# Performance work log

Measured on AMD Instinct MI355X. Metric: run time of the kernel, lower is better.

The kernel has to match this reference:

```python
import jax, jax.numpy as jnp
import numpy as np

QN, QP = -8.0, 7.0  # int4: Qn=-2**3, Qp=2**3-1
LOG2E = 1.4426950408889634  # 1/ln(2)

def round_ste(x):
    return x + jax.lax.stop_gradient(jnp.round(x) - x)

def sg(x):
    return jax.lax.stop_gradient(x)

def mean_var_int(x_int, scale=1024):
    """Serial integer running-mean/var recurrence over the last dim.
    x_int: (B,H,N,D) int32. Returns mu (int values, float32) and varn float32, shape (B,H,N,1).
    Matches the torch loop: m_i = m_{i-1} + (x_i-m_{i-1})*int(1024/(i+1))//1024,
    v_i = v_{i-1} + (x_i-m_{i-1})*(x_i-m_i), with m_0=x_0, v_0=0 (same as the general
    recurrence with m_{-1}=v_{-1}=0 since int(1024/1)=1024)."""
    D = x_int.shape[3]
    coef = jnp.array([scale // (i + 1) for i in range(D)], dtype=jnp.int32)
    xt = jnp.moveaxis(x_int, 3, 0)  # (D,B,H,N)
    z = jnp.zeros(x_int.shape[:3], jnp.int32)
    def step(carry, inp):
        m, v = carry
        xi, c = inp
        d = xi - m
        new_m = m + (d * c) // scale  # floor division, matches torch //
        new_v = v + d * (xi - new_m)
        return (new_m, new_v), None
    (m, v), _ = jax.lax.scan(step, (z, z), (xt, coef))
    mu = m[..., None].astype(jnp.float32)
    varn = v[..., None].astype(jnp.float32) / D
    return mu, varn

def q_attention_forward(x0, qkv_w, qkv_b, qkv_alpha, qkv_act_alpha,
                        proj_w, proj_b, proj_alpha, proj_act_alpha,
                        norm_q_w, norm_q_b, norm_k_w, norm_k_b,
                        q_alpha, k_alpha, v_alpha, attn_alpha,
                        num_heads=12):
    B, N, C = x0.shape
    H = num_heads
    hd = C // H
    head_scale = hd ** -0.5

    # input activation quantization (ActQ_v2 then .int())
    a_in = qkv_act_alpha.mean()
    x0_2b = sg(jnp.round(jnp.clip(x0 / a_in, QN, QP)))  # int-valued (B,N,C)

    # int4 qkv weight quantization (per-output-channel alpha), integer GEMM
    w_qkv = sg(jnp.round(jnp.clip(qkv_w / qkv_alpha[:, None], QN, QP)))  # (3C,C)
    qkv = jnp.einsum('bnc,oc->bno', x0_2b, w_qkv)
    bias_i = sg(jnp.trunc(qkv_b / a_in / qkv_alpha))  # bias.int()
    qkv = qkv + bias_i

    qkv = jnp.transpose(qkv.reshape(B, N, 3, H, hd), (2, 0, 3, 1, 4))
    q0, k0, v0 = qkv[0], qkv[1], qkv[2]  # (B,H,N,hd)
    alpha_r = qkv_alpha.reshape(3, H, 1, hd)

    # q branch: scaled integer mean/var norm + scaled quantization
    xq = q0 * alpha_r[0]
    mu_q, var_q = mean_var_int(xq.astype(jnp.int32))
    q1 = (xq - mu_q) / (jnp.sqrt(var_q) + 1e-5)
    aq = q_alpha.mean()
    q2 = sg(jnp.round(jnp.clip((q1 + norm_q_b / norm_q_w) * norm_q_w / aq, QN, QP)))

    # k branch
    xk = k0 * alpha_r[1]
    mu_k, var_k = mean_var_int(xk.astype(jnp.int32))
    k1 = (xk - mu_k) / (jnp.sqrt(var_k) + 1e-5)
    ak = k_alpha.mean()
    k2 = sg(jnp.round(jnp.clip((k1 + norm_k_b / norm_k_w) * norm_k_w / ak, QN, QP)))

    # v branch
    av = v_alpha.mean()
    v2 = sg(jnp.round(jnp.clip(v0 * (a_in * alpha_r[2]) / av, QN, QP)))

    # integer q @ k^T
    qk = jnp.einsum('bhqd,bhkd->bhqk', q2, k2)  # (B,H,N,N)

    # power-of-two softmax approximation: 2^floor(e) * (1 + frac(e))
    s = head_scale * aq * ak
    e = LOG2E * s * qk
    f = jnp.floor(e)
    attn_exp = jnp.exp2(f) * (1.0 + (e - f))
    am = attn_alpha.mean()
    attn_norm = attn_exp / attn_exp.sum(-1, keepdims=True)
    attn2 = sg(jnp.round(jnp.clip(attn_norm / am, QN, QP)))

    x1p = jnp.einsum('bhqk,bhkd->bhqd', attn2, v2)
    x1p = jnp.transpose(x1p, (0, 2, 1, 3)).reshape(B, N, C)

    # proj-act quantization (round_pass STE, no .int() here in torch)
    ap = proj_act_alpha.mean()
    x1_2b = round_ste(jnp.clip(x1p * (am * av) / ap, QN, QP))

    w_p = sg(jnp.round(jnp.clip(proj_w / proj_alpha[:, None], QN, QP)))  # w_q.int()
    x2 = jnp.einsum('bnc,oc->bno', x1_2b, w_p) * proj_alpha * ap + proj_b
    return x2

def setup_inputs() -> dict:
    key = jax.random.key(0)
    ks = jax.random.split(key, 17)
    B, N, C, H = 4, 1024, 768, 12
    u = lambda k, shape, lo, hi: jax.random.uniform(k, shape, jnp.float32, lo, hi)
    return {
        "x0": jax.random.normal(ks[0], (B, N, C), jnp.float32),
        "qkv_w": jax.random.normal(ks[1], (3 * C, C), jnp.float32) * 0.02,
        "qkv_b": jax.random.normal(ks[2], (3 * C,), jnp.float32),
        "qkv_alpha": u(ks[3], (3 * C,), 0.008, 0.012),
        "qkv_act_alpha": u(ks[4], (C,), 0.25, 0.35),
        "proj_w": jax.random.normal(ks[5], (C, C), jnp.float32) * 0.02,
        "proj_b": jax.random.normal(ks[6], (C,), jnp.float32) * 0.02,
        "proj_alpha": u(ks[7], (C,), 0.008, 0.012),
        "proj_act_alpha": u(ks[8], (C,), 0.008, 0.012),
        "norm_q_w": u(ks[9], (C // H,), 0.8, 1.2),
        "norm_q_b": jax.random.normal(ks[10], (C // H,), jnp.float32) * 0.1,
        "norm_k_w": u(ks[11], (C // H,), 0.8, 1.2),
        "norm_k_b": jax.random.normal(ks[12], (C // H,), jnp.float32) * 0.1,
        "q_alpha": u(ks[13], (H,), 0.25, 0.35),
        "k_alpha": u(ks[14], (H,), 0.25, 0.35),
        "v_alpha": u(ks[15], (H,), 0.15, 0.25),
        "attn_alpha": u(ks[16], (H,), 0.0008, 0.0015),
    }

def reference(x0, qkv_w, qkv_b, qkv_alpha, qkv_act_alpha,
              proj_w, proj_b, proj_alpha, proj_act_alpha,
              norm_q_w, norm_q_b, norm_k_w, norm_k_b,
              q_alpha, k_alpha, v_alpha, attn_alpha):
    return q_attention_forward(x0, qkv_w, qkv_b, qkv_alpha, qkv_act_alpha,
                               proj_w, proj_b, proj_alpha, proj_act_alpha,
                               norm_q_w, norm_q_b, norm_k_w, norm_k_b,
                               q_alpha, k_alpha, v_alpha, attn_alpha)
```

## Files before the change

### kernel.cpp

```cpp
#include <hip/hip_runtime.h>

typedef unsigned short u16;
typedef unsigned int u32;
typedef __attribute__((ext_vector_type(8))) u16 u16x8;
typedef __attribute__((ext_vector_type(8))) __bf16 bf16x8;
typedef __attribute__((ext_vector_type(4))) float f32x4;

#define LOG2E_F 1.4426950408889634f

__device__ __forceinline__ u16 f2bf(float f) {
  return (u16)(__float_as_uint(f) >> 16);
}
__device__ __forceinline__ float clip87(float x) {
  return fminf(fmaxf(x, -8.0f), 7.0f);
}

typedef const __attribute__((address_space(1))) u32* gp32;
typedef __attribute__((address_space(3))) u32* lp32;
__device__ __forceinline__ void gl16(const void* g, void* l) {
  __builtin_amdgcn_global_load_lds((gp32)g, (lp32)l, 16, 0, 0);
}

__global__ void k_scalars(const float* __restrict__ qkv_act_alpha,
                          const float* __restrict__ proj_act_alpha,
                          const float* __restrict__ q_alpha,
                          const float* __restrict__ k_alpha,
                          const float* __restrict__ v_alpha,
                          const float* __restrict__ attn_alpha,
                          float* __restrict__ scal) {
  int tid = threadIdx.x;
  int wave = tid >> 6, lane = tid & 63;
  if (wave < 6) {
    const float* src = nullptr; int n = 0;
    switch (wave) {
      case 0: src = qkv_act_alpha;  n = 768; break;
      case 1: src = q_alpha;        n = 12;  break;
      case 2: src = k_alpha;        n = 12;  break;
      case 3: src = v_alpha;        n = 12;  break;
      case 4: src = attn_alpha;     n = 12;  break;
      case 5: src = proj_act_alpha; n = 768; break;
    }
    double s = 0.0;
    for (int i = lane; i < n; i += 64) s += (double)src[i];
    s += __shfl_xor(s, 1);
    s += __shfl_xor(s, 2);
    s += __shfl_xor(s, 4);
    s += __shfl_xor(s, 8);
    s += __shfl_xor(s, 16);
    s += __shfl_xor(s, 32);
    if (lane == 0) scal[wave] = (float)(s / (double)n);
  }
  __syncthreads();
  if (tid == 0) {
    float aq = scal[1], ak = scal[2];
    float s_ = (0.125f * aq) * ak;
    scal[6] = LOG2E_F * s_;
    scal[7] = scal[4] * scal[3];
  }
}

__global__ __launch_bounds__(256) void k_quant_weights(
    const float* __restrict__ qkv_w, const float* __restrict__ qkv_alpha,
    const float* __restrict__ qkv_b, const float* __restrict__ proj_w,
    const float* __restrict__ proj_alpha, const float* __restrict__ scal,
    u16* __restrict__ wq, u16* __restrict__ wp, float* __restrict__ biasi) {
  int idx = blockIdx.x * 256 + threadIdx.x;
  const int T1 = 2304 * 768, T2 = 768 * 768;
  if (idx < T1) {
    int o = idx / 768;
    wq[idx] = f2bf(rintf(clip87(qkv_w[idx] / qkv_alpha[o])));
  } else if (idx < T1 + T2) {
    int j = idx - T1;
    int o = j / 768;
    wp[j] = f2bf(rintf(clip87(proj_w[j] / proj_alpha[o])));
  } else if (idx < T1 + T2 + 2304) {
    int o = idx - T1 - T2;
    biasi[o] = truncf((qkv_b[o] / scal[0]) / qkv_alpha[o]);
  }
}

__global__ __launch_bounds__(256) void k_quant_x0(const float* __restrict__ x0,
                                                  const float* __restrict__ scal,
                                                  u16* __restrict__ x0q) {
  int base = (blockIdx.x * 256 + threadIdx.x) * 8;
  float a = scal[0];
  f32x4 v0 = *(const f32x4*)&x0[base];
  f32x4 v1 = *(const f32x4*)&x0[base + 4];
  u16x8 o;
  #pragma unroll
  for (int j = 0; j < 4; j++) o[j] = f2bf(rintf(clip87(v0[j] / a)));
  #pragma unroll
  for (int j = 0; j < 4; j++) o[4 + j] = f2bf(rintf(clip87(v1[j] / a)));
  *(u16x8*)&x0q[base] = o;
}

__global__ __launch_bounds__(256) void k_gemm_qkv(
    const u16* __restrict__ A, const u16* __restrict__ Bt,
    const float* __restrict__ biasi, const float* __restrict__ qkv_alpha,
    const float* __restrict__ nqw, const float* __restrict__ nqb,
    const float* __restrict__ nkw, const float* __restrict__ nkb,
    const float* __restrict__ scal,
    u16* __restrict__ q2, u16* __restrict__ k2, u16* __restrict__ v2t) {
  const int K = 768;
  __shared__ __align__(16) float xt[128 * 129];
  u16* lA = (u16*)xt;
  u16* lB = ((u16*)xt) + 128 * 32;
  int tid = threadIdx.x;
  int lane = tid & 63, wave = tid >> 6;
  int wr = wave >> 1, wc = wave & 1;
  int m0 = blockIdx.y * 128, n0 = blockIdx.x * 128;

  f32x4 acc[4][4];
  #pragma unroll
  for (int mi = 0; mi < 4; mi++)
    #pragma unroll
    for (int ni = 0; ni < 4; ni++) acc[mi][ni] = (f32x4){0.f, 0.f, 0.f, 0.f};

  int srow = wave * 32 + (lane >> 2);
  int scol = (lane & 3) * 8;
  const u16* gA = A + (size_t)(m0 + srow) * K + scol;
  const u16* gB = Bt + (size_t)(n0 + srow) * K + scol;
  u16* lA0 = lA + wave * 2 * 512;
  u16* lB0 = lB + wave * 2 * 512;
  const size_t rowskip = (size_t)16 * K;

  int arow = wr * 64 + (lane & 15);
  int brow = wc * 64 + (lane & 15);
  int acol = (lane >> 4) * 8;

  for (int k0 = 0; k0 < K; k0 += 32) {
    gl16(gA + k0, lA0);
    gl16(gA + k0 + rowskip, lA0 + 512);
    gl16(gB + k0, lB0);
    gl16(gB + k0 + rowskip, lB0 + 512);
    __syncthreads();
    bf16x8 af[4], bf[4];
    #pragma unroll
    for (int mi = 0; mi < 4; mi++) af[mi] = *(const bf16x8*)&lA[(arow + mi * 16) * 32 + acol];
    #pragma unroll
    for (int ni = 0; ni < 4; ni++) bf[ni] = *(const bf16x8*)&lB[(brow + ni * 16) * 32 + acol];
    #pragma unroll
    for (int mi = 0; mi < 4; mi++)
      #pragma unroll
      for (int ni = 0; ni < 4; ni++)
        acc[mi][ni] = __builtin_amdgcn_mfma_f32_16x16x32_bf16(af[mi], bf[ni], acc[mi][ni], 0, 0, 0);
    __syncthreads();
  }

  int lrow = (lane >> 4) * 4, lcol = lane & 15;
  #pragma unroll
  for (int mi = 0; mi < 4; mi++)
    #pragma unroll
    for (int ni = 0; ni < 4; ni++) {
      int c = wc * 64 + ni * 16 + lcol;
      float bs = biasi[n0 + c];
      #pragma unroll
      for (int rr = 0; rr < 4; rr++) {
        int r = wr * 64 + mi * 16 + lrow + rr;
        xt[r * 129 + c] = acc[mi][ni][rr] + bs;
      }
    }
  __syncthreads();

  int branch = blockIdx.x / 6, hp = blockIdx.x % 6;
  int b = m0 >> 10, nb = m0 & 1023;
  if (branch == 2) {
    int c = tid & 127, hf = tid >> 7;
    int h = hp * 2 + (c >> 6), d = c & 63;
    float av = scal[3];
    float coefv = scal[0] * qkv_alpha[1536 + h * 64 + d];
    u16* dst = v2t + ((size_t)(b * 12 + h) * 64 + d) * 1024 + nb + hf * 64;
    #pragma unroll
    for (int g = 0; g < 8; g++) {
      u16x8 t8;
      #pragma unroll
      for (int j = 0; j < 8; j++) {
        float val = xt[(hf * 64 + g * 8 + j) * 129 + c];
        t8[j] = f2bf(rintf(clip87((val * coefv) / av)));
      }
      *(u16x8*)(dst + g * 8) = t8;
    }
  } else {
    int r = tid & 127, hs = tid >> 7;
    int h = hp * 2 + hs;
    const float* alph = qkv_alpha + branch * 768 + h * 64;
    const float* wv = branch == 0 ? nqw : nkw;
    const float* bv = branch == 0 ? nqb : nkb;
    float as = branch == 0 ? scal[1] : scal[2];
    float xq[64];
    #pragma unroll
    for (int d = 0; d < 64; d++) xq[d] = xt[r * 129 + hs * 64 + d] * alph[d];
    int m = 0, v = 0;
    #pragma unroll
    for (int i = 0; i < 64; i++) {
      int xi = (int)xq[i];
      int dd = xi - m;
      m += (dd * (1024 / (i + 1))) >> 10;
      v += dd * (xi - m);
    }
    float muf = (float)m;
    float den = sqrtf((float)v * 0.015625f) + 1e-5f;
    u16* outp = (branch == 0 ? q2 : k2) + ((size_t)(b * 12 + h) * 1024 + nb + r) * 64;
    #pragma unroll
    for (int g = 0; g < 8; g++) {
      u16x8 t8;
      #pragma unroll
      for (int j = 0; j < 8; j++) {
        int d = g * 8 + j;
        float q1 = (xq[d] - muf) / den;
        float bw = bv[d] / wv[d];
        float t = (q1 + bw) * wv[d] / as;
        t8[j] = f2bf(rintf(clip87(t)));
      }
      *(u16x8*)(outp + g * 8) = t8;
    }
  }
}

__global__ __launch_bounds__(256) void k_gemm_proj(
    const u16* __restrict__ A, const u16* __restrict__ Bt,
    float* __restrict__ Cout, const float* __restrict__ palpha,
    const float* __restrict__ pbias, const float* __restrict__ scal) {
  const int K = 768, N = 768;
  __shared__ __align__(16) u16 lA[128 * 32];
  __shared__ __align__(16) u16 lB[128 * 32];
  int tid = threadIdx.x;
  int lane = tid & 63, wave = tid >> 6;
  int wr = wave >> 1, wc = wave & 1;
  int m0 = blockIdx.y * 128, n0 = blockIdx.x * 128;

  f32x4 acc[4][4];
  #pragma unroll
  for (int mi = 0; mi < 4; mi++)
    #pragma unroll
    for (int ni = 0; ni < 4; ni++) acc[mi][ni] = (f32x4){0.f, 0.f, 0.f, 0.f};

  int srow = wave * 32 + (lane >> 2);
  int scol = (lane & 3) * 8;
  const u16* gA = A + (size_t)(m0 + srow) * K + scol;
  const u16* gB = Bt + (size_t)(n0 + srow) * K + scol;
  u16* lA0 = lA + wave * 2 * 512;
  u16* lB0 = lB + wave * 2 * 512;
  const size_t rowskip = (size_t)16 * K;

  int arow = wr * 64 + (lane & 15);
  int brow = wc * 64 + (lane & 15);
  int acol = (lane >> 4) * 8;

  for (int k0 = 0; k0 < K; k0 += 32) {
    gl16(gA + k0, lA0);
    gl16(gA + k0 + rowskip, lA0 + 512);
    gl16(gB + k0, lB0);
    gl16(gB + k0 + rowskip, lB0 + 512);
    __syncthreads();
    bf16x8 af[4], bf[4];
    #pragma unroll
    for (int mi = 0; mi < 4; mi++) af[mi] = *(const bf16x8*)&lA[(arow + mi * 16) * 32 + acol];
    #pragma unroll
    for (int ni = 0; ni < 4; ni++) bf[ni] = *(const bf16x8*)&lB[(brow + ni * 16) * 32 + acol];
    #pragma unroll
    for (int mi = 0; mi < 4; mi++)
      #pragma unroll
      for (int ni = 0; ni < 4; ni++)
        acc[mi][ni] = __builtin_amdgcn_mfma_f32_16x16x32_bf16(af[mi], bf[ni], acc[mi][ni], 0, 0, 0);
    __syncthreads();
  }

  int lrow = (lane >> 4) * 4, lcol = lane & 15;
  float ap = scal[5];
  #pragma unroll
  for (int mi = 0; mi < 4; mi++)
    #pragma unroll
    for (int ni = 0; ni < 4; ni++) {
      int col = n0 + wc * 64 + ni * 16 + lcol;
      float pa = palpha[col], pb = pbias[col];
      #pragma unroll
      for (int rr = 0; rr < 4; rr++) {
        int row = m0 + wr * 64 + mi * 16 + lrow + rr;
        Cout[(size_t)row * N + col] = (acc[mi][ni][rr] * pa) * ap + pb;
      }
    }
}

__global__ __launch_bounds__(256) void k_attn(
    const u16* __restrict__ q2, const u16* __restrict__ k2,
    const u16* __restrict__ v2t, const float* __restrict__ scal,
    u16* __restrict__ x1q) {
  __shared__ __align__(16) u16 lK[64 * 72];
  __shared__ __align__(16) u16 lV[64 * 72];
  __shared__ __align__(16) u16 lP[64 * 72];
  __shared__ float rs_lds[64];
  int tid = threadIdx.x, lane = tid & 63, wave = tid >> 6;
  int qt = blockIdx.x, bh = blockIdx.y;
  const float escale = scal[6], am = scal[4], am_av = scal[7], apc = scal[5];

  size_t qrow = (size_t)bh * 1024 + qt * 64 + wave * 16 + (lane & 15);
  bf16x8 qf0 = *(const bf16x8*)(q2 + qrow * 64 + (lane >> 4) * 8);
  bf16x8 qf1 = *(const bf16x8*)(q2 + qrow * 64 + 32 + (lane >> 4) * 8);

  const u16* k2b = k2 + (size_t)bh * 1024 * 64;
  const u16* v2b = v2t + (size_t)bh * 64 * 1024;
  int sr = tid >> 2, sc = (tid & 3) * 16;

  double rsum[4] = {0.0, 0.0, 0.0, 0.0};
  for (int kt = 0; kt < 16; kt++) {
    const u16* src = k2b + (size_t)(kt * 64 + sr) * 64 + sc;
    *(u16x8*)&lK[sr * 72 + sc]     = *(const u16x8*)src;
    *(u16x8*)&lK[sr * 72 + sc + 8] = *(const u16x8*)(src + 8);
    __syncthreads();
    float part[4] = {0.f, 0.f, 0.f, 0.f};
    #pragma unroll
    for (int ct = 0; ct < 4; ct++) {
      bf16x8 kf0 = *(const bf16x8*)&lK[(ct * 16 + (lane & 15)) * 72 + (lane >> 4) * 8];
      bf16x8 kf1 = *(const bf16x8*)&lK[(ct * 16 + (lane & 15)) * 72 + 32 + (lane >> 4) * 8];
      f32x4 s = {0.f, 0.f, 0.f, 0.f};
      s = __builtin_amdgcn_mfma_f32_16x16x32_bf16(qf0, kf0, s, 0, 0, 0);
      s = __builtin_amdgcn_mfma_f32_16x16x32_bf16(qf1, kf1, s, 0, 0, 0);
      #pragma unroll
      for (int rr = 0; rr < 4; rr++) {
        float e = escale * s[rr];
        float f = floorf(e);
        float pe = ldexpf(1.0f + (e - f), (int)f);
        part[rr] += pe;
      }
    }
    #pragma unroll
    for (int rr = 0; rr < 4; rr++) rsum[rr] += (double)part[rr];
    __syncthreads();
  }
  #pragma unroll
  for (int rr = 0; rr < 4; rr++) {
    double s = rsum[rr];
    s += __shfl_xor(s, 1);
    s += __shfl_xor(s, 2);
    s += __shfl_xor(s, 4);
    s += __shfl_xor(s, 8);
    if ((lane & 15) == 0) rs_lds[wave * 16 + (lane >> 4) * 4 + rr] = (float)s;
  }
  __syncthreads();
  float fac[4];
  #pragma unroll
  for (int rr = 0; rr < 4; rr++)
    fac[rr] = 1.0f / (rs_lds[wave * 16 + (lane >> 4) * 4 + rr] * am);

  f32x4 accv[4];
  #pragma unroll
  for (int ct = 0; ct < 4; ct++) accv[ct] = (f32x4){0.f, 0.f, 0.f, 0.f};

  for (int kt = 0; kt < 16; kt++) {
    const u16* srcK = k2b + (size_t)(kt * 64 + sr) * 64 + sc;
    *(u16x8*)&lK[sr * 72 + sc]     = *(const u16x8*)srcK;
    *(u16x8*)&lK[sr * 72 + sc + 8] = *(const u16x8*)(srcK + 8);
    const u16* srcV = v2b + (size_t)sr * 1024 + kt * 64 + sc;
    *(u16x8*)&lV[sr * 72 + sc]     = *(const u16x8*)srcV;
    *(u16x8*)&lV[sr * 72 + sc + 8] = *(const u16x8*)(srcV + 8);
    __syncthreads();
    #pragma unroll
    for (int ct = 0; ct < 4; ct++) {
      bf16x8 kf0 = *(const bf16x8*)&lK[(ct * 16 + (lane & 15)) * 72 + (lane >> 4) * 8];
      bf16x8 kf1 = *(const bf16x8*)&lK[(ct * 16 + (lane & 15)) * 72 + 32 + (lane >> 4) * 8];
      f32x4 s = {0.f, 0.f, 0.f, 0.f};
      s = __builtin_amdgcn_mfma_f32_16x16x32_bf16(qf0, kf0, s, 0, 0, 0);
      s = __builtin_amdgcn_mfma_f32_16x16x32_bf16(qf1, kf1, s, 0, 0, 0);
      #pragma unroll
      for (int rr = 0; rr < 4; rr++) {
        float e = escale * s[rr];
        float f = floorf(e);
        float pe = ldexpf(1.0f + (e - f), (int)f);
        float a2 = rintf(fminf(pe * fac[rr], 7.0f));
        lP[(wave * 16 + (lane >> 4) * 4 + rr) * 72 + ct * 16 + (lane & 15)] = f2bf(a2);
      }
    }
    __syncthreads();
    bf16x8 pf0 = *(const bf16x8*)&lP[(wave * 16 + (lane & 15)) * 72 + (lane >> 4) * 8];
    bf16x8 pf1 = *(const bf16x8*)&lP[(wave * 16 + (lane & 15)) * 72 + 32 + (lane >> 4) * 8];
    #pragma unroll
    for (int ct = 0; ct < 4; ct++) {
      bf16x8 vf0 = *(const bf16x8*)&lV[(ct * 16 + (lane & 15)) * 72 + (lane >> 4) * 8];
      bf16x8 vf1 = *(const bf16x8*)&lV[(ct * 16 + (lane & 15)) * 72 + 32 + (lane >> 4) * 8];
      accv[ct] = __builtin_amdgcn_mfma_f32_16x16x32_bf16(pf0, vf0, accv[ct], 0, 0, 0);
      accv[ct] = __builtin_amdgcn_mfma_f32_16x16x32_bf16(pf1, vf1, accv[ct], 0, 0, 0);
    }
    __syncthreads();
  }

  int b = bh / 12, h = bh % 12;
  #pragma unroll
  for (int ct = 0; ct < 4; ct++)
    #pragma unroll
    for (int rr = 0; rr < 4; rr++) {
      int qr = qt * 64 + wave * 16 + (lane >> 4) * 4 + rr;
      int col = h * 64 + ct * 16 + (lane & 15);
      float t = (accv[ct][rr] * am_av) / apc;
      x1q[((size_t)b * 1024 + qr) * 768 + col] = f2bf(rintf(clip87(t)));
    }
}

extern "C" void kernel_launch(void* const* d_in, const int* in_sizes, int n_in,
                              void* d_out, int out_size, void* d_ws, size_t ws_size,
                              hipStream_t stream) {
  const float* x0             = (const float*)d_in[0];
  const float* qkv_w          = (const float*)d_in[1];
  const float* qkv_b          = (const float*)d_in[2];
  const float* qkv_alpha      = (const float*)d_in[3];
  const float* qkv_act_alpha  = (const float*)d_in[4];
  const float* proj_w         = (const float*)d_in[5];
  const float* proj_b         = (const float*)d_in[6];
  const float* proj_alpha     = (const float*)d_in[7];
  const float* proj_act_alpha = (const float*)d_in[8];
  const float* nqw            = (const float*)d_in[9];
  const float* nqb            = (const float*)d_in[10];
  const float* nkw            = (const float*)d_in[11];
  const float* nkb            = (const float*)d_in[12];
  const float* q_alpha        = (const float*)d_in[13];
  const float* k_alpha        = (const float*)d_in[14];
  const float* v_alpha        = (const float*)d_in[15];
  const float* attn_alpha     = (const float*)d_in[16];
  float* out = (float*)d_out;

  char* ws = (char*)d_ws;
  size_t off = 0;
  auto alloc = [&](size_t bytes) -> void* {
    off = (off + 255) & ~(size_t)255;
    void* p = ws + off;
    off += bytes;
    return p;
  };
  float* scal = (float*)alloc(64);
  u16* wq     = (u16*)alloc((size_t)2304 * 768 * 2);
  u16* wp     = (u16*)alloc((size_t)768 * 768 * 2);
  float* biasi= (float*)alloc((size_t)2304 * 4);
  u16* x0q    = (u16*)alloc((size_t)4096 * 768 * 2);
  u16* q2     = (u16*)alloc((size_t)48 * 1024 * 64 * 2);
  u16* k2     = (u16*)alloc((size_t)48 * 1024 * 64 * 2);
  u16* v2t    = (u16*)alloc((size_t)48 * 1024 * 64 * 2);
  u16* x1q    = (u16*)alloc((size_t)4096 * 768 * 2);

  k_scalars<<<1, 384, 0, stream>>>(qkv_act_alpha, proj_act_alpha, q_alpha, k_alpha,
                                   v_alpha, attn_alpha, scal);

  int totW = 2304 * 768 + 768 * 768 + 2304;
  k_quant_weights<<<(totW + 255) / 256, 256, 0, stream>>>(qkv_w, qkv_alpha, qkv_b,
                                                          proj_w, proj_alpha, scal,
                                                          wq, wp, biasi);

  k_quant_x0<<<(4096 * 768) / (256 * 8), 256, 0, stream>>>(x0, scal, x0q);

  k_gemm_qkv<<<dim3(18, 32), 256, 0, stream>>>(x0q, wq, biasi, qkv_alpha,
                                               nqw, nqb, nkw, nkb, scal,
                                               q2, k2, v2t);

  k_attn<<<dim3(16, 48), 256, 0, stream>>>(q2, k2, v2t, scal, x1q);

  k_gemm_proj<<<dim3(6, 32), 256, 0, stream>>>(x1q, wp, out, proj_alpha, proj_b, scal);
}
```

Baseline: 228.9 us.

## Double-buffer GEMM tiles with BK=64 and XOR-swizzled LDS layout

Replaces the single-buffer BK=32 GEMM main loop in both the qkv and proj kernels with a shared helper. The helper stages 64-wide K tiles into two LDS buffers so the next tile loads while the current one feeds MFMA. It XOR-swizzles column chunks to reduce LDS bank conflicts and halves the number of barriers per K. The proj kernel now allocates 64KB of LDS, which can lower occupancy.

```diff
diff --git a/kernel.cpp b/kernel.cpp
--- a/kernel.cpp
+++ b/kernel.cpp
@@ -94,6 +94,59 @@
   *(u16x8*)&x0q[base] = o;
 }
 
+#define BUF_A(c) (smem_u16 + (c) * 8192)
+#define BUF_B(c) (smem_u16 + 16384 + (c) * 8192)
+
+__device__ __forceinline__ void stage_tile(const u16* gAl, const u16* gBl, int K,
+                                           u16* bufA, u16* bufB, int w) {
+  #pragma unroll
+  for (int i = 0; i < 4; i++)
+    gl16(gAl + (size_t)(i * 8) * K, bufA + (w * 32 + i * 8) * 64);
+  #pragma unroll
+  for (int i = 0; i < 4; i++)
+    gl16(gBl + (size_t)(i * 8) * K, bufB + (w * 32 + i * 8) * 64);
+}
+
+__device__ __forceinline__ void gemm_steps(const u16* __restrict__ A,
+                                           const u16* __restrict__ Bt, int K,
+                                           int m0, int n0, u16* smem_u16,
+                                           int lane, int wave, f32x4 acc[4][4]) {
+  int rsub = lane >> 3;
+  int jsrc = (lane & 7) ^ rsub;
+  const u16* gAl = A + (size_t)(m0 + wave * 32 + rsub) * K + jsrc * 8;
+  const u16* gBl = Bt + (size_t)(n0 + wave * 32 + rsub) * K + jsrc * 8;
+
+  int arow = (wave >> 1) * 64 + (lane & 15);
+  int brow = (wave & 1) * 64 + (lane & 15);
+  int nsteps = K / 64;
+
+  stage_tile(gAl, gBl, K, BUF_A(0), BUF_B(0), wave);
+  __syncthreads();
+  for (int t = 0; t < nsteps; t++) {
+    int cur = t & 1;
+    if (t + 1 < nsteps)
+      stage_tile(gAl + (t + 1) * 64, gBl + (t + 1) * 64, K,
+                 BUF_A(cur ^ 1), BUF_B(cur ^ 1), wave);
+    const u16* bA = BUF_A(cur);
+    const u16* bB = BUF_B(cur);
+    #pragma unroll
+    for (int kk = 0; kk < 2; kk++) {
+      int jj = ((kk * 4 + (lane >> 4)) ^ (lane & 7)) * 8;
+      bf16x8 af[4], bf[4];
+      #pragma unroll
+      for (int mi = 0; mi < 4; mi++) af[mi] = *(const bf16x8*)&bA[(arow + mi * 16) * 64 + jj];
+      #pragma unroll
+      for (int ni = 0; ni < 4; ni++) bf[ni] = *(const bf16x8*)&bB[(brow + ni * 16) * 64 + jj];
+      #pragma unroll
+      for (int mi = 0; mi < 4; mi++)
+        #pragma unroll
+        for (int ni = 0; ni < 4; ni++)
+          acc[mi][ni] = __builtin_amdgcn_mfma_f32_16x16x32_bf16(af[mi], bf[ni], acc[mi][ni], 0, 0, 0);
+    }
+    __syncthreads();
+  }
+}
+
 __global__ __launch_bounds__(256) void k_gemm_qkv(
     const u16* __restrict__ A, const u16* __restrict__ Bt,
     const float* __restrict__ biasi, const float* __restrict__ qkv_alpha,
@@ -102,9 +155,9 @@
     const float* __restrict__ scal,
     u16* __restrict__ q2, u16* __restrict__ k2, u16* __restrict__ v2t) {
   const int K = 768;
-  __shared__ __align__(16) float xt[128 * 129];
-  u16* lA = (u16*)xt;
-  u16* lB = ((u16*)xt) + 128 * 32;
+  __shared__ __align__(16) char smem[128 * 129 * 4];
+  u16* smem_u16 = (u16*)smem;
+  float* xt = (float*)smem;
   int tid = threadIdx.x;
   int lane = tid & 63, wave = tid >> 6;
   int wr = wave >> 1, wc = wave & 1;
@@ -116,36 +169,7 @@
     #pragma unroll
     for (int ni = 0; ni < 4; ni++) acc[mi][ni] = (f32x4){0.f, 0.f, 0.f, 0.f};
 
-  int srow = wave * 32 + (lane >> 2);
-  int scol = (lane & 3) * 8;
-  const u16* gA = A + (size_t)(m0 + srow) * K + scol;
-  const u16* gB = Bt + (size_t)(n0 + srow) * K + scol;
-  u16* lA0 = lA + wave * 2 * 512;
-  u16* lB0 = lB + wave * 2 * 512;
-  const size_t rowskip = (size_t)16 * K;
-
-  int arow = wr * 64 + (lane & 15);
-  int brow = wc * 64 + (lane & 15);
-  int acol = (lane >> 4) * 8;
-
-  for (int k0 = 0; k0 < K; k0 += 32) {
-    gl16(gA + k0, lA0);
-    gl16(gA + k0 + rowskip, lA0 + 512);
-    gl16(gB + k0, lB0);
-    gl16(gB + k0 + rowskip, lB0 + 512);
-    __syncthreads();
-    bf16x8 af[4], bf[4];
-    #pragma unroll
-    for (int mi = 0; mi < 4; mi++) af[mi] = *(const bf16x8*)&lA[(arow + mi * 16) * 32 + acol];
-    #pragma unroll
-    for (int ni = 0; ni < 4; ni++) bf[ni] = *(const bf16x8*)&lB[(brow + ni * 16) * 32 + acol];
-    #pragma unroll
-    for (int mi = 0; mi < 4; mi++)
-      #pragma unroll
-      for (int ni = 0; ni < 4; ni++)
-        acc[mi][ni] = __builtin_amdgcn_mfma_f32_16x16x32_bf16(af[mi], bf[ni], acc[mi][ni], 0, 0, 0);
-    __syncthreads();
-  }
+  gemm_steps(A, Bt, K, m0, n0, smem_u16, lane, wave, acc);
 
   int lrow = (lane >> 4) * 4, lcol = lane & 15;
   #pragma unroll
@@ -222,8 +246,8 @@
     float* __restrict__ Cout, const float* __restrict__ palpha,
     const float* __restrict__ pbias, const float* __restrict__ scal) {
   const int K = 768, N = 768;
-  __shared__ __align__(16) u16 lA[128 * 32];
-  __shared__ __align__(16) u16 lB[128 * 32];
+  __shared__ __align__(16) char smem[65536];
+  u16* smem_u16 = (u16*)smem;
   int tid = threadIdx.x;
   int lane = tid & 63, wave = tid >> 6;
   int wr = wave >> 1, wc = wave & 1;
@@ -235,36 +259,7 @@
     #pragma unroll
     for (int ni = 0; ni < 4; ni++) acc[mi][ni] = (f32x4){0.f, 0.f, 0.f, 0.f};
 
-  int srow = wave * 32 + (lane >> 2);
-  int scol = (lane & 3) * 8;
-  const u16* gA = A + (size_t)(m0 + srow) * K + scol;
-  const u16* gB = Bt + (size_t)(n0 + srow) * K + scol;
-  u16* lA0 = lA + wave * 2 * 512;
-  u16* lB0 = lB + wave * 2 * 512;
-  const size_t rowskip = (size_t)16 * K;
-
-  int arow = wr * 64 + (lane & 15);
-  int brow = wc * 64 + (lane & 15);
-  int acol = (lane >> 4) * 8;
-
-  for (int k0 = 0; k0 < K; k0 += 32) {
-    gl16(gA + k0, lA0);
-    gl16(gA + k0 + rowskip, lA0 + 512);
-    gl16(gB + k0, lB0);
-    gl16(gB + k0 + rowskip, lB0 + 512);
-    __syncthreads();
-    bf16x8 af[4], bf[4];
-    #pragma unroll
-    for (int mi = 0; mi < 4; mi++) af[mi] = *(const bf16x8*)&lA[(arow + mi * 16) * 32 + acol];
-    #pragma unroll
-    for (int ni = 0; ni < 4; ni++) bf[ni] = *(const bf16x8*)&lB[(brow + ni * 16) * 32 + acol];
-    #pragma unroll
-    for (int mi = 0; mi < 4; mi++)
-      #pragma unroll
-      for (int ni = 0; ni < 4; ni++)
-        acc[mi][ni] = __builtin_amdgcn_mfma_f32_16x16x32_bf16(af[mi], bf[ni], acc[mi][ni], 0, 0, 0);
-    __syncthreads();
-  }
+  gemm_steps(A, Bt, K, m0, n0, smem_u16, lane, wave, acc);
 
   int lrow = (lane >> 4) * 4, lcol = lane & 15;
   float ap = scal[5];
```

Result: faster. 212.7 us (-7.1%).
